# Performance work log

Hardware: AMD Instinct MI355X
Metric: run time of the kernel (lower is better)

The kernel has to match this reference:

```python
import jax, jax.numpy as jnp
import numpy as np

N_NODES = 100000
N_EDGES = 1600000
D_FEAT = 256
HIDDEN = 256
N_CLASSES = 64


def gcn_conv(x, edge_index, W, b, num_nodes):
    """PyG GCNConv: h = W x; add self loops; symmetric D^-1/2 (A+I) D^-1/2 aggregation; + bias."""
    h = x @ W  # [N, out]
    loop = jnp.arange(num_nodes, dtype=edge_index.dtype)
    row = jnp.concatenate([edge_index[0], loop])  # source nodes
    col = jnp.concatenate([edge_index[1], loop])  # target nodes
    deg = jax.ops.segment_sum(jnp.ones_like(col, dtype=h.dtype), col, num_segments=num_nodes)
    dinv = jnp.where(deg > 0, jax.lax.rsqrt(deg), 0.0)
    norm = dinv[row] * dinv[col]  # per-edge normalization
    out = jax.ops.segment_sum(h[row] * norm[:, None], col, num_segments=num_nodes)
    return out + b


def setup_inputs() -> dict:
    key = jax.random.key(0)
    k1, k2, k3, k4 = jax.random.split(key, 4)
    x = jax.random.normal(k1, (N_NODES, D_FEAT), dtype=jnp.float32)
    edge_index = jax.random.randint(k2, (2, N_EDGES), 0, N_NODES, dtype=jnp.int64)
    W1 = jax.random.normal(k3, (D_FEAT, HIDDEN), dtype=jnp.float32) * (1.0 / np.sqrt(D_FEAT))
    b1 = jnp.zeros((HIDDEN,), dtype=jnp.float32)
    W2 = jax.random.normal(k4, (HIDDEN, N_CLASSES), dtype=jnp.float32) * (1.0 / np.sqrt(HIDDEN))
    b2 = jnp.zeros((N_CLASSES,), dtype=jnp.float32)
    return {"x": x, "edge_index": edge_index, "W1": W1, "b1": b1, "W2": W2, "b2": b2}


def reference(x, edge_index, W1, b1, W2, b2):
    # conv1 -> relu -> dropout (eval mode: identity) -> conv2
    h = gcn_conv(x, edge_index, W1, b1, N_NODES)
    h = jax.nn.relu(h)
    out = gcn_conv(h, edge_index, W2, b2, N_NODES)  # [N, num_classes]
    return out
```

## Files before the change

kernel.cpp:

```cpp
#include <hip/hip_runtime.h>
#include <hip/hip_bf16.h>

#define N_NODES 100000
#define N_PAD   100032
#define N_EDGES 1600000
#define D_FEAT 256
#define HIDDEN 256
#define N_CLASSES 64

#define NBKT 391
#define TILE 4096
#define CAP  8192

typedef __attribute__((ext_vector_type(8))) short bf16x8;
typedef __attribute__((ext_vector_type(4))) float f32x4;

__device__ inline float b2f(ushort u) {
    unsigned v = ((unsigned)u) << 16;
    float f; __builtin_memcpy(&f, &v, 4); return f;
}
__device__ inline ushort f2b(float f) {
    unsigned u; __builtin_memcpy(&u, &f, 4);
    unsigned r = (u + 0x7fffu + ((u >> 16) & 1u)) >> 16;
    return (ushort)r;
}

__global__ __launch_bounds__(256)
void zero_bcnt(int* bcnt) {
    int i = blockIdx.x * 256 + threadIdx.x;
    if (i < NBKT) bcnt[i] = 0;
}

__global__ __launch_bounds__(256)
void bin_count(const int* __restrict__ cols, int* bcnt, int nE) {
    __shared__ int h[NBKT];
    int t = threadIdx.x;
    for (int i = t; i < NBKT; i += 256) h[i] = 0;
    __syncthreads();
    for (long e = (long)blockIdx.x * 256 + t; e < nE; e += (long)gridDim.x * 256)
        atomicAdd(&h[cols[e] >> 8], 1);
    __syncthreads();
    for (int i = t; i < NBKT; i += 256)
        if (h[i]) atomicAdd(&bcnt[i], h[i]);
}

__global__ __launch_bounds__(256)
void bucket_scan(const int* __restrict__ bcnt, int* __restrict__ bbase,
                 int* __restrict__ bcur, int* __restrict__ offsets) {
    __shared__ int sd[256];
    int t = threadIdx.x;
    int i0 = 2 * t, i1 = 2 * t + 1;
    int a = (i0 < NBKT) ? bcnt[i0] : 0;
    int b = (i1 < NBKT) ? bcnt[i1] : 0;
    int s = a + b;
    sd[t] = s; __syncthreads();
    #pragma unroll
    for (int off = 1; off < 256; off <<= 1) {
        int v = (t >= off) ? sd[t - off] : 0;
        __syncthreads();
        sd[t] += v;
        __syncthreads();
    }
    int ex = sd[t] - s;
    if (i0 <= NBKT) bbase[i0] = ex;
    if (i0 < NBKT)  bcur[i0] = ex;
    if (i1 <= NBKT) bbase[i1] = ex + a;
    if (i1 < NBKT)  bcur[i1] = ex + a;
    if (t == 0) offsets[N_NODES] = N_EDGES;
}

__global__ __launch_bounds__(256)
void bin_scatter(const int* __restrict__ rows, const int* __restrict__ cols,
                 int* bcur, unsigned* __restrict__ bins, int nE)
{
    __shared__ unsigned recs[TILE];
    __shared__ ushort bos[TILE];
    __shared__ int hist[NBKT], excl[NBKT], cursor[NBKT], gbase[NBKT];
    __shared__ int sd[256];
    int t = threadIdx.x;
    long e0 = (long)blockIdx.x * TILE;
    int cnt = (int)min((long)TILE, (long)nE - e0);
    for (int i = t; i < NBKT; i += 256) hist[i] = 0;
    __syncthreads();
    int myrow[TILE / 256], mycol[TILE / 256];
    #pragma unroll
    for (int k = 0; k < TILE / 256; ++k) {
        int i = k * 256 + t;
        if (i < cnt) {
            myrow[k] = rows[e0 + i];
            mycol[k] = cols[e0 + i];
            atomicAdd(&hist[mycol[k] >> 8], 1);
        }
    }
    __syncthreads();
    {
        int i0 = 2 * t, i1 = 2 * t + 1;
        int a = (i0 < NBKT) ? hist[i0] : 0;
        int b = (i1 < NBKT) ? hist[i1] : 0;
        int s = a + b;
        sd[t] = s; __syncthreads();
        #pragma unroll
        for (int off = 1; off < 256; off <<= 1) {
            int v = (t >= off) ? sd[t - off] : 0;
            __syncthreads();
            sd[t] += v;
            __syncthreads();
        }
        int ex = sd[t] - s;
        if (i0 < NBKT) { excl[i0] = ex;     cursor[i0] = ex; }
        if (i1 < NBKT) { excl[i1] = ex + a; cursor[i1] = ex + a; }
    }
    __syncthreads();
    #pragma unroll
    for (int k = 0; k < TILE / 256; ++k) {
        int i = k * 256 + t;
        if (i < cnt) {
            int b = mycol[k] >> 8;
            int s = atomicAdd(&cursor[b], 1);
            recs[s] = ((unsigned)(mycol[k] & 255) << 24) | (unsigned)myrow[k];
            bos[s] = (ushort)b;
        }
    }
    __syncthreads();
    for (int i = t; i < NBKT; i += 256)
        if (hist[i] > 0) gbase[i] = atomicAdd(&bcur[i], hist[i]);
    __syncthreads();
    for (int i = t; i < cnt; i += 256) {
        int b = bos[i];
        bins[gbase[b] + (i - excl[b])] = recs[i];
    }
}

__global__ __launch_bounds__(256)
void bucket_fill(const unsigned* __restrict__ bins, const int* __restrict__ bbase,
                 int* __restrict__ offsets, float* __restrict__ dinv,
                 int* __restrict__ esrc)
{
    int b = blockIdx.x, t = threadIdx.x;
    int s0 = bbase[b], s1 = bbase[b + 1];
    int len = s1 - s0;
    __shared__ int cnt[256];
    __shared__ int sd[256];
    __shared__ int cur[256];
    __shared__ int stage[CAP];
    cnt[t] = 0;
    __syncthreads();
    for (int i = t; i < len; i += 256) atomicAdd(&cnt[bins[s0 + i] >> 24], 1);
    __syncthreads();
    int c = cnt[t];
    sd[t] = c; __syncthreads();
    #pragma unroll
    for (int off = 1; off < 256; off <<= 1) {
        int v = (t >= off) ? sd[t - off] : 0;
        __syncthreads();
        sd[t] += v;
        __syncthreads();
    }
    int ex = sd[t] - c;
    cur[t] = ex;
    int node = b * 256 + t;
    if (node < N_NODES) {
        offsets[node] = s0 + ex;
        dinv[node] = rsqrtf(1.0f + (float)c);
    }
    __syncthreads();
    if (len <= CAP) {
        for (int i = t; i < len; i += 256) {
            unsigned r = bins[s0 + i];
            int p = atomicAdd(&cur[r >> 24], 1);
            stage[p] = (int)(r & 0xFFFFFFu);
        }
        __syncthreads();
        for (int i = t; i < len; i += 256) esrc[s0 + i] = stage[i];
    } else {
        for (int i = t; i < len; i += 256) {
            unsigned r = bins[s0 + i];
            int p = atomicAdd(&cur[r >> 24], 1);
            esrc[s0 + p] = (int)(r & 0xFFFFFFu);
        }
    }
}

__global__ __launch_bounds__(256)
void split_x(const float* __restrict__ x, ushort* __restrict__ xh, ushort* __restrict__ xl) {
    int i = blockIdx.x * 256 + threadIdx.x;
    if (i >= N_NODES * D_FEAT / 4) return;
    float4 v = ((const float4*)x)[i];
    ushort4 h, l;
    h.x = f2b(v.x); l.x = f2b(v.x - b2f(h.x));
    h.y = f2b(v.y); l.y = f2b(v.y - b2f(h.y));
    h.z = f2b(v.z); l.z = f2b(v.z - b2f(h.z));
    h.w = f2b(v.w); l.w = f2b(v.w - b2f(h.w));
    ((ushort4*)xh)[i] = h;
    ((ushort4*)xl)[i] = l;
}

__global__ __launch_bounds__(256)
void fragw1(const float* __restrict__ W1, ushort* __restrict__ wfh, ushort* __restrict__ wfl) {
    int t = blockIdx.x * 256 + threadIdx.x;
    int ks = t >> 10, nb = (t >> 6) & 15, lane = t & 63;
    int m = lane & 15, quad = lane >> 4;
    ushort h8[8], l8[8];
    #pragma unroll
    for (int j = 0; j < 8; ++j) {
        int k = ks * 32 + quad * 8 + j;
        float w = W1[k * HIDDEN + nb * 16 + m];
        h8[j] = f2b(w);
        l8[j] = f2b(w - b2f(h8[j]));
    }
    long off = ((long)(ks * 16 + nb) * 64 + lane) * 8;
    *(ushort4*)&wfh[off]     = make_ushort4(h8[0], h8[1], h8[2], h8[3]);
    *(ushort4*)&wfh[off + 4] = make_ushort4(h8[4], h8[5], h8[6], h8[7]);
    *(ushort4*)&wfl[off]     = make_ushort4(l8[0], l8[1], l8[2], l8[3]);
    *(ushort4*)&wfl[off + 4] = make_ushort4(l8[4], l8[5], l8[6], l8[7]);
}

__global__ __launch_bounds__(256)
void fragw2(const float* __restrict__ W2, ushort* __restrict__ wf) {
    int t = blockIdx.x * 256 + threadIdx.x;
    int ks = t >> 8, nb = (t >> 6) & 3, lane = t & 63;
    int m = lane & 15, quad = lane >> 4;
    ushort h8[8];
    #pragma unroll
    for (int j = 0; j < 8; ++j) {
        int k = ks * 32 + quad * 8 + j;
        h8[j] = f2b(W2[k * N_CLASSES + nb * 16 + m]);
    }
    long off = ((long)(ks * 4 + nb) * 64 + lane) * 8;
    *(ushort4*)&wf[off]     = make_ushort4(h8[0], h8[1], h8[2], h8[3]);
    *(ushort4*)&wf[off + 4] = make_ushort4(h8[4], h8[5], h8[6], h8[7]);
}

__global__ __launch_bounds__(256)
void gemm1_mfma(const ushort* __restrict__ xh, const ushort* __restrict__ xl,
                const ushort* __restrict__ wfh, const ushort* __restrict__ wfl,
                const float* __restrict__ dinv, ushort* __restrict__ hs)
{
    int tid = threadIdx.x;
    int lane = tid & 63;
    int wm = (tid >> 6) & 1;
    int wn = tid >> 7;
    int row0 = blockIdx.y * 128 + wm * 64;
    int nb0 = blockIdx.x * 8 + wn * 4;
    int m = lane & 15, quad = lane >> 4;

    f32x4 acc[4][4];
    #pragma unroll
    for (int i = 0; i < 4; ++i)
        #pragma unroll
        for (int j = 0; j < 4; ++j) acc[i][j] = (f32x4){0.f, 0.f, 0.f, 0.f};

    for (int ks = 0; ks < 8; ++ks) {
        bf16x8 ah[4], al[4];
        #pragma unroll
        for (int mf = 0; mf < 4; ++mf) {
            long r = (long)(row0 + mf * 16 + m);
            ah[mf] = *(const bf16x8*)(xh + r * D_FEAT + ks * 32 + quad * 8);
            al[mf] = *(const bf16x8*)(xl + r * D_FEAT + ks * 32 + quad * 8);
        }
        #pragma unroll
        for (int nbl = 0; nbl < 4; ++nbl) {
            long boff = ((long)(ks * 16 + nb0 + nbl) * 64 + lane) * 8;
            bf16x8 bh = *(const bf16x8*)(wfh + boff);
            bf16x8 bl = *(const bf16x8*)(wfl + boff);
            #pragma unroll
            for (int mf = 0; mf < 4; ++mf) {
                acc[mf][nbl] = __builtin_amdgcn_mfma_f32_16x16x32_bf16(ah[mf], bh, acc[mf][nbl], 0, 0, 0);
                acc[mf][nbl] = __builtin_amdgcn_mfma_f32_16x16x32_bf16(ah[mf], bl, acc[mf][nbl], 0, 0, 0);
                acc[mf][nbl] = __builtin_amdgcn_mfma_f32_16x16x32_bf16(al[mf], bh, acc[mf][nbl], 0, 0, 0);
            }
        }
    }

    #pragma unroll
    for (int mf = 0; mf < 4; ++mf)
        #pragma unroll
        for (int reg = 0; reg < 4; ++reg) {
            int row = row0 + mf * 16 + quad * 4 + reg;
            if (row < N_NODES) {
                float dv = dinv[row];
                #pragma unroll
                for (int nbl = 0; nbl < 4; ++nbl)
                    hs[(long)row * HIDDEN + (nb0 + nbl) * 16 + m] = f2b(acc[mf][nbl][reg] * dv);
            }
        }
}

__global__ __launch_bounds__(256)
void gemm2_mfma(const ushort* __restrict__ r1s, const ushort* __restrict__ wf,
                ushort* __restrict__ h2)
{
    int tid = threadIdx.x;
    int wv = tid >> 6, lane = tid & 63;
    int row0 = blockIdx.x * 256 + wv * 64;
    int m = lane & 15, quad = lane >> 4;

    f32x4 acc[4][4];
    #pragma unroll
    for (int i = 0; i < 4; ++i)
        #pragma unroll
        for (int j = 0; j < 4; ++j) acc[i][j] = (f32x4){0.f, 0.f, 0.f, 0.f};

    for (int ks = 0; ks < 8; ++ks) {
        bf16x8 a[4];
        #pragma unroll
        for (int mf = 0; mf < 4; ++mf) {
            long r = (long)(row0 + mf * 16 + m);
            a[mf] = *(const bf16x8*)(r1s + r * HIDDEN + ks * 32 + quad * 8);
        }
        #pragma unroll
        for (int nb = 0; nb < 4; ++nb) {
            bf16x8 b = *(const bf16x8*)(wf + ((long)(ks * 4 + nb) * 64 + lane) * 8);
            #pragma unroll
            for (int mf = 0; mf < 4; ++mf)
                acc[mf][nb] = __builtin_amdgcn_mfma_f32_16x16x32_bf16(a[mf], b, acc[mf][nb], 0, 0, 0);
        }
    }

    #pragma unroll
    for (int mf = 0; mf < 4; ++mf)
        #pragma unroll
        for (int reg = 0; reg < 4; ++reg) {
            int row = row0 + mf * 16 + quad * 4 + reg;
            if (row < N_NODES) {
                #pragma unroll
                for (int nb = 0; nb < 4; ++nb)
                    h2[(long)row * N_CLASSES + nb * 16 + m] = f2b(acc[mf][nb][reg]);
            }
        }
}

__global__ __launch_bounds__(256)
void agg256(const ushort* __restrict__ src, const int* __restrict__ offsets,
            const int* __restrict__ esrc, const float* __restrict__ dinv,
            const float* __restrict__ b1, ushort* __restrict__ dst)
{
    int wave = threadIdx.x >> 6, lane = threadIdx.x & 63;
    int v = blockIdx.x * 4 + wave;
    int c = lane << 2;
    ushort4 s = *(const ushort4*)&src[(long)v * 256 + c];
    float a0 = b2f(s.x), a1 = b2f(s.y), a2 = b2f(s.z), a3 = b2f(s.w);
    int e = offsets[v], end = offsets[v + 1];
    for (; e + 4 <= end; e += 4) {
        int s0 = esrc[e], s1 = esrc[e + 1], s2 = esrc[e + 2], s3 = esrc[e + 3];
        ushort4 u0 = *(const ushort4*)&src[(long)s0 * 256 + c];
        ushort4 u1 = *(const ushort4*)&src[(long)s1 * 256 + c];
        ushort4 u2 = *(const ushort4*)&src[(long)s2 * 256 + c];
        ushort4 u3 = *(const ushort4*)&src[(long)s3 * 256 + c];
        a0 += (b2f(u0.x) + b2f(u1.x)) + (b2f(u2.x) + b2f(u3.x));
        a1 += (b2f(u0.y) + b2f(u1.y)) + (b2f(u2.y) + b2f(u3.y));
        a2 += (b2f(u0.z) + b2f(u1.z)) + (b2f(u2.z) + b2f(u3.z));
        a3 += (b2f(u0.w) + b2f(u1.w)) + (b2f(u2.w) + b2f(u3.w));
    }
    for (; e < end; ++e) {
        ushort4 u = *(const ushort4*)&src[(long)esrc[e] * 256 + c];
        a0 += b2f(u.x); a1 += b2f(u.y); a2 += b2f(u.z); a3 += b2f(u.w);
    }
    float dv = dinv[v];
    float4 bb = *(const float4*)&b1[c];
    float r0 = dv * fmaxf(fmaf(dv, a0, bb.x), 0.f);
    float r1 = dv * fmaxf(fmaf(dv, a1, bb.y), 0.f);
    float r2 = dv * fmaxf(fmaf(dv, a2, bb.z), 0.f);
    float r3 = dv * fmaxf(fmaf(dv, a3, bb.w), 0.f);
    *(ushort4*)&dst[(long)v * 256 + c] = make_ushort4(f2b(r0), f2b(r1), f2b(r2), f2b(r3));
}

__global__ __launch_bounds__(256)
void agg64b(const ushort* __restrict__ src, const int* __restrict__ offsets,
            const int* __restrict__ esrc, const float* __restrict__ dinv,
            const float* __restrict__ b2, float* __restrict__ out)
{
    int wave = threadIdx.x >> 6, lane = threadIdx.x & 63;
    int v = blockIdx.x * 4 + wave;
    float acc = b2f(src[(long)v * 64 + lane]);
    int e = offsets[v], end = offsets[v + 1];
    for (; e + 4 <= end; e += 4) {
        int s0 = esrc[e], s1 = esrc[e + 1], s2 = esrc[e + 2], s3 = esrc[e + 3];
        float a0 = b2f(src[(long)s0 * 64 + lane]);
        float a1 = b2f(src[(long)s1 * 64 + lane]);
        float a2 = b2f(src[(long)s2 * 64 + lane]);
        float a3 = b2f(src[(long)s3 * 64 + lane]);
        acc += (a0 + a1) + (a2 + a3);
    }
    for (; e < end; ++e) acc += b2f(src[(long)esrc[e] * 64 + lane]);
    out[(long)v * 64 + lane] = fmaf(dinv[v], acc, b2[lane]);
}

#define WS_DINV   0UL
#define WS_OFFS   524288UL
#define WS_BCNT   1048576UL
#define WS_BBASE  1052672UL
#define WS_BCUR   1056768UL
#define WS_ESRC   1064960UL
#define WS_BINS   7602176UL
#define WS_XH     20447232UL
#define WS_XL     71663616UL
#define WS_WF1H   122880000UL
#define WS_WF1L   123011072UL
#define WS_WF2    123142144UL
#define WS_HS1    123174912UL

extern "C" void kernel_launch(void* const* d_in, const int* in_sizes, int n_in,
                              void* d_out, int out_size, void* d_ws, size_t ws_size,
                              hipStream_t stream)
{
    const float* x  = (const float*)d_in[0];
    const int*   ei = (const int*)d_in[1];
    const float* W1 = (const float*)d_in[2];
    const float* b1 = (const float*)d_in[3];
    const float* W2 = (const float*)d_in[4];
    const float* b2 = (const float*)d_in[5];
    float* out = (float*)d_out;

    const int* rows = ei;
    const int* cols = ei + N_EDGES;

    char* ws = (char*)d_ws;
    float*    dinv    = (float*)(ws + WS_DINV);
    int*      offsets = (int*)(ws + WS_OFFS);
    int*      bcnt    = (int*)(ws + WS_BCNT);
    int*      bbase   = (int*)(ws + WS_BBASE);
    int*      bcur    = (int*)(ws + WS_BCUR);
    int*      esrc    = (int*)(ws + WS_ESRC);
    unsigned* bins    = (unsigned*)(ws + WS_BINS);
    ushort*   xh      = (ushort*)(ws + WS_XH);
    ushort*   xl      = (ushort*)(ws + WS_XL);
    ushort*   wf1h    = (ushort*)(ws + WS_WF1H);
    ushort*   wf1l    = (ushort*)(ws + WS_WF1L);
    ushort*   wf2     = (ushort*)(ws + WS_WF2);
    ushort*   hs1     = (ushort*)(ws + WS_HS1);
    ushort*   r1s     = xl;
    ushort*   h2      = xh;

    zero_bcnt<<<2, 256, 0, stream>>>(bcnt);
    bin_count<<<512, 256, 0, stream>>>(cols, bcnt, N_EDGES);
    bucket_scan<<<1, 256, 0, stream>>>(bcnt, bbase, bcur, offsets);
    bin_scatter<<<(N_EDGES + TILE - 1) / TILE, 256, 0, stream>>>(rows, cols, bcur, bins, N_EDGES);
    bucket_fill<<<NBKT, 256, 0, stream>>>(bins, bbase, offsets, dinv, esrc);

    split_x<<<(N_NODES * D_FEAT / 4 + 255) / 256, 256, 0, stream>>>(x, xh, xl);
    fragw1<<<32, 256, 0, stream>>>(W1, wf1h, wf1l);
    fragw2<<<8, 256, 0, stream>>>(W2, wf2);

    const int agg_grid = N_NODES / 4;

    {
        dim3 g1(2, (N_NODES + 127) / 128);
        gemm1_mfma<<<g1, 256, 0, stream>>>(xh, xl, wf1h, wf1l, dinv, hs1);
    }
    agg256<<<agg_grid, 256, 0, stream>>>(hs1, offsets, esrc, dinv, b1, r1s);

    gemm2_mfma<<<(N_NODES + 255) / 256, 256, 0, stream>>>(r1s, wf2, h2);
    agg64b<<<agg_grid, 256, 0, stream>>>(h2, offsets, esrc, dinv, b2, out);
}
```

Baseline: 511.7 us.

## Fuse fp32-to-bf16 hi/lo split into GEMM1 and merge weight-prep kernels

Removes the separate split_x pass, so GEMM1 reads fp32 x directly and forms the bf16 hi/lo halves in registers. The hi half is now a truncation rather than a rounding, with the residual carried in the lo half. This drops a full write and re-read of two 51 MB bf16 copies of x, but GEMM1 now reads twice the bytes of x per tile, and those reads are duplicated across the two column blocks. The two weight-fragment kernels are merged into one launch, and both aggregation kernels issue 8 gathers per iteration instead of 4 for more memory-level parallelism.

```diff
diff --git a/kernel.cpp b/kernel.cpp
--- a/kernel.cpp
+++ b/kernel.cpp
@@ -2,7 +2,6 @@
 #include <hip/hip_bf16.h>
 
 #define N_NODES 100000
-#define N_PAD   100032
 #define N_EDGES 1600000
 #define D_FEAT 256
 #define HIDDEN 256
@@ -182,57 +181,44 @@
 }
 
 __global__ __launch_bounds__(256)
-void split_x(const float* __restrict__ x, ushort* __restrict__ xh, ushort* __restrict__ xl) {
-    int i = blockIdx.x * 256 + threadIdx.x;
-    if (i >= N_NODES * D_FEAT / 4) return;
-    float4 v = ((const float4*)x)[i];
-    ushort4 h, l;
-    h.x = f2b(v.x); l.x = f2b(v.x - b2f(h.x));
-    h.y = f2b(v.y); l.y = f2b(v.y - b2f(h.y));
-    h.z = f2b(v.z); l.z = f2b(v.z - b2f(h.z));
-    h.w = f2b(v.w); l.w = f2b(v.w - b2f(h.w));
-    ((ushort4*)xh)[i] = h;
-    ((ushort4*)xl)[i] = l;
-}
-
-__global__ __launch_bounds__(256)
-void fragw1(const float* __restrict__ W1, ushort* __restrict__ wfh, ushort* __restrict__ wfl) {
+void fragw(const float* __restrict__ W1, ushort* __restrict__ wfh,
+           ushort* __restrict__ wfl,
+           const float* __restrict__ W2, ushort* __restrict__ wf2) {
     int t = blockIdx.x * 256 + threadIdx.x;
-    int ks = t >> 10, nb = (t >> 6) & 15, lane = t & 63;
+    int lane = t & 63;
     int m = lane & 15, quad = lane >> 4;
-    ushort h8[8], l8[8];
-    #pragma unroll
-    for (int j = 0; j < 8; ++j) {
-        int k = ks * 32 + quad * 8 + j;
-        float w = W1[k * HIDDEN + nb * 16 + m];
-        h8[j] = f2b(w);
-        l8[j] = f2b(w - b2f(h8[j]));
-    }
-    long off = ((long)(ks * 16 + nb) * 64 + lane) * 8;
-    *(ushort4*)&wfh[off]     = make_ushort4(h8[0], h8[1], h8[2], h8[3]);
-    *(ushort4*)&wfh[off + 4] = make_ushort4(h8[4], h8[5], h8[6], h8[7]);
-    *(ushort4*)&wfl[off]     = make_ushort4(l8[0], l8[1], l8[2], l8[3]);
-    *(ushort4*)&wfl[off + 4] = make_ushort4(l8[4], l8[5], l8[6], l8[7]);
-}
-
-__global__ __launch_bounds__(256)
-void fragw2(const float* __restrict__ W2, ushort* __restrict__ wf) {
-    int t = blockIdx.x * 256 + threadIdx.x;
-    int ks = t >> 8, nb = (t >> 6) & 3, lane = t & 63;
-    int m = lane & 15, quad = lane >> 4;
-    ushort h8[8];
-    #pragma unroll
-    for (int j = 0; j < 8; ++j) {
-        int k = ks * 32 + quad * 8 + j;
-        h8[j] = f2b(W2[k * N_CLASSES + nb * 16 + m]);
-    }
-    long off = ((long)(ks * 4 + nb) * 64 + lane) * 8;
-    *(ushort4*)&wf[off]     = make_ushort4(h8[0], h8[1], h8[2], h8[3]);
-    *(ushort4*)&wf[off + 4] = make_ushort4(h8[4], h8[5], h8[6], h8[7]);
-}
-
-__global__ __launch_bounds__(256)
-void gemm1_mfma(const ushort* __restrict__ xh, const ushort* __restrict__ xl,
+    if (t < 8192) {
+        int ks = t >> 10, nb = (t >> 6) & 15;
+        ushort h8[8], l8[8];
+        #pragma unroll
+        for (int j = 0; j < 8; ++j) {
+            int k = ks * 32 + quad * 8 + j;
+            float w = W1[k * HIDDEN + nb * 16 + m];
+            h8[j] = f2b(w);
+            l8[j] = f2b(w - b2f(h8[j]));
+        }
+        long off = ((long)(ks * 16 + nb) * 64 + lane) * 8;
+        *(ushort4*)&wfh[off]     = make_ushort4(h8[0], h8[1], h8[2], h8[3]);
+        *(ushort4*)&wfh[off + 4] = make_ushort4(h8[4], h8[5], h8[6], h8[7]);
+        *(ushort4*)&wfl[off]     = make_ushort4(l8[0], l8[1], l8[2], l8[3]);
+        *(ushort4*)&wfl[off + 4] = make_ushort4(l8[4], l8[5], l8[6], l8[7]);
+    } else {
+        int u = t - 8192;
+        int ks = u >> 8, nb = (u >> 6) & 3;
+        ushort h8[8];
+        #pragma unroll
+        for (int j = 0; j < 8; ++j) {
+            int k = ks * 32 + quad * 8 + j;
+            h8[j] = f2b(W2[k * N_CLASSES + nb * 16 + m]);
+        }
+        long off = ((long)(ks * 4 + nb) * 64 + lane) * 8;
+        *(ushort4*)&wf2[off]     = make_ushort4(h8[0], h8[1], h8[2], h8[3]);
+        *(ushort4*)&wf2[off + 4] = make_ushort4(h8[4], h8[5], h8[6], h8[7]);
+    }
+}
+
+__global__ __launch_bounds__(256)
+void gemm1_mfma(const float* __restrict__ x,
                 const ushort* __restrict__ wfh, const ushort* __restrict__ wfl,
                 const float* __restrict__ dinv, ushort* __restrict__ hs)
 {
@@ -254,9 +240,21 @@
         bf16x8 ah[4], al[4];
         #pragma unroll
         for (int mf = 0; mf < 4; ++mf) {
-            long r = (long)(row0 + mf * 16 + m);
-            ah[mf] = *(const bf16x8*)(xh + r * D_FEAT + ks * 32 + quad * 8);
-            al[mf] = *(const bf16x8*)(xl + r * D_FEAT + ks * 32 + quad * 8);
+            int rr = row0 + mf * 16 + m;
+            rr = (rr < N_NODES) ? rr : (N_NODES - 1);
+            const float* p = x + (long)rr * D_FEAT + ks * 32 + quad * 8;
+            float4 v0 = *(const float4*)p;
+            float4 v1 = *(const float4*)(p + 4);
+            float vv[8] = {v0.x, v0.y, v0.z, v0.w, v1.x, v1.y, v1.z, v1.w};
+            #pragma unroll
+            for (int j = 0; j < 8; ++j) {
+                unsigned u; __builtin_memcpy(&u, &vv[j], 4);
+                ushort hh = (ushort)(u >> 16);
+                float hv = b2f(hh);
+                ushort ll = f2b(vv[j] - hv);
+                ah[mf][j] = (short)hh;
+                al[mf][j] = (short)ll;
+            }
         }
         #pragma unroll
         for (int nbl = 0; nbl < 4; ++nbl) {
@@ -341,16 +339,16 @@
     ushort4 s = *(const ushort4*)&src[(long)v * 256 + c];
     float a0 = b2f(s.x), a1 = b2f(s.y), a2 = b2f(s.z), a3 = b2f(s.w);
     int e = offsets[v], end = offsets[v + 1];
-    for (; e + 4 <= end; e += 4) {
-        int s0 = esrc[e], s1 = esrc[e + 1], s2 = esrc[e + 2], s3 = esrc[e + 3];
-        ushort4 u0 = *(const ushort4*)&src[(long)s0 * 256 + c];
-        ushort4 u1 = *(const ushort4*)&src[(long)s1 * 256 + c];
-        ushort4 u2 = *(const ushort4*)&src[(long)s2 * 256 + c];
-        ushort4 u3 = *(const ushort4*)&src[(long)s3 * 256 + c];
-        a0 += (b2f(u0.x) + b2f(u1.x)) + (b2f(u2.x) + b2f(u3.x));
-        a1 += (b2f(u0.y) + b2f(u1.y)) + (b2f(u2.y) + b2f(u3.y));
-        a2 += (b2f(u0.z) + b2f(u1.z)) + (b2f(u2.z) + b2f(u3.z));
-        a3 += (b2f(u0.w) + b2f(u1.w)) + (b2f(u2.w) + b2f(u3.w));
+    for (; e + 8 <= end; e += 8) {
+        ushort4 u[8];
+        #pragma unroll
+        for (int j = 0; j < 8; ++j)
+            u[j] = *(const ushort4*)&src[(long)esrc[e + j] * 256 + c];
+        #pragma unroll
+        for (int j = 0; j < 8; ++j) {
+            a0 += b2f(u[j].x); a1 += b2f(u[j].y);
+            a2 += b2f(u[j].z); a3 += b2f(u[j].w);
+        }
     }
     for (; e < end; ++e) {
         ushort4 u = *(const ushort4*)&src[(long)esrc[e] * 256 + c];
@@ -374,13 +372,12 @@
     int v = blockIdx.x * 4 + wave;
     float acc = b2f(src[(long)v * 64 + lane]);
     int e = offsets[v], end = offsets[v + 1];
-    for (; e + 4 <= end; e += 4) {
-        int s0 = esrc[e], s1 = esrc[e + 1], s2 = esrc[e + 2], s3 = esrc[e + 3];
-        float a0 = b2f(src[(long)s0 * 64 + lane]);
-        float a1 = b2f(src[(long)s1 * 64 + lane]);
-        float a2 = b2f(src[(long)s2 * 64 + lane]);
-        float a3 = b2f(src[(long)s3 * 64 + lane]);
-        acc += (a0 + a1) + (a2 + a3);
+    for (; e + 8 <= end; e += 8) {
+        float a[8];
+        #pragma unroll
+        for (int j = 0; j < 8; ++j)
+            a[j] = b2f(src[(long)esrc[e + j] * 64 + lane]);
+        acc += ((a[0] + a[1]) + (a[2] + a[3])) + ((a[4] + a[5]) + (a[6] + a[7]));
     }
     for (; e < end; ++e) acc += b2f(src[(long)esrc[e] * 64 + lane]);
     out[(long)v * 64 + lane] = fmaf(dinv[v], acc, b2[lane]);
@@ -393,8 +390,8 @@
 #define WS_BCUR   1056768UL
 #define WS_ESRC   1064960UL
 #define WS_BINS   7602176UL
-#define WS_XH     20447232UL
-#define WS_XL     71663616UL
+#define WS_H2     20447232UL
+#define WS_R1S    71663616UL
 #define WS_WF1H   122880000UL
 #define WS_WF1L   123011072UL
 #define WS_WF2    123142144UL
@@ -423,14 +420,12 @@
     int*      bcur    = (int*)(ws + WS_BCUR);
     int*      esrc    = (int*)(ws + WS_ESRC);
     unsigned* bins    = (unsigned*)(ws + WS_BINS);
-    ushort*   xh      = (ushort*)(ws + WS_XH);
-    ushort*   xl      = (ushort*)(ws + WS_XL);
+    ushort*   h2      = (ushort*)(ws + WS_H2);
+    ushort*   r1s     = (ushort*)(ws + WS_R1S);
     ushort*   wf1h    = (ushort*)(ws + WS_WF1H);
     ushort*   wf1l    = (ushort*)(ws + WS_WF1L);
     ushort*   wf2     = (ushort*)(ws + WS_WF2);
     ushort*   hs1     = (ushort*)(ws + WS_HS1);
-    ushort*   r1s     = xl;
-    ushort*   h2      = xh;
 
     zero_bcnt<<<2, 256, 0, stream>>>(bcnt);
     bin_count<<<512, 256, 0, stream>>>(cols, bcnt, N_EDGES);
@@ -438,15 +433,13 @@
     bin_scatter<<<(N_EDGES + TILE - 1) / TILE, 256, 0, stream>>>(rows, cols, bcur, bins, N_EDGES);
     bucket_fill<<<NBKT, 256, 0, stream>>>(bins, bbase, offsets, dinv, esrc);
 
-    split_x<<<(N_NODES * D_FEAT / 4 + 255) / 256, 256, 0, stream>>>(x, xh, xl);
-    fragw1<<<32, 256, 0, stream>>>(W1, wf1h, wf1l);
-    fragw2<<<8, 256, 0, stream>>>(W2, wf2);
+    fragw<<<40, 256, 0, stream>>>(W1, wf1h, wf1l, W2, wf2);
 
     const int agg_grid = N_NODES / 4;
 
     {
         dim3 g1(2, (N_NODES + 127) / 128);
-        gemm1_mfma<<<g1, 256, 0, stream>>>(xh, xl, wf1h, wf1l, dinv, hs1);
+        gemm1_mfma<<<g1, 256, 0, stream>>>(x, wf1h, wf1l, dinv, hs1);
     }
     agg256<<<agg_grid, 256, 0, stream>>>(hs1, offsets, esrc, dinv, b1, r1s);
 
```

New measurement: 494.1 us. 3.4% less time.
